# Kernel optimization log

Hardware: AMD Instinct MI355X
Metric: run time of the kernel (lower is better)

## Reference

```python
import jax, jax.numpy as jnp
import numpy as np
from jax.ops import segment_sum

N = 100000      # nodes
E = 1600000     # edges
G = 128         # graphs in batch
D = 128         # input (embedding) dim
H = 128         # hidden dim
WALK = 16       # random-walk length
PED = 16        # PE embed dim
L = 5           # GNN layers
OUT = 10        # classes
EPS = 1e-5      # batchnorm eps


def setup_inputs() -> dict:
    key = jax.random.key(0)
    ks = jax.random.split(key, 32)
    f = lambda k, shp: (jax.random.normal(k, shp, dtype=jnp.float32) * 0.05)
    inp = {
        'x': jnp.zeros((N,), dtype=jnp.int64) if jax.config.jax_enable_x64 else jnp.zeros((N,), dtype=jnp.int32),
        'edge_index': jax.random.randint(ks[0], (2, E), 0, N),
        'batch': jnp.sort(jax.random.randint(ks[1], (N,), 0, G)),
        'emb_table': f(ks[2], (1, D)),
        'pe_w': f(ks[3], (WALK, PED)), 'pe_b': f(ks[4], (PED,)),
        'proj_w': f(ks[5], (D + PED, H)), 'proj_b': f(ks[6], (H,)),
        'gin_w1': f(ks[7], (L, H, H)), 'gin_b1': f(ks[8], (L, H)),
        'gin_w2': f(ks[9], (L, H, H)), 'gin_b2': f(ks[10], (L, H)),
        'bn_g': jnp.ones((L, H), jnp.float32), 'bn_b': jnp.zeros((L, H), jnp.float32),
        'ffn_w1': f(ks[11], (L, H, 2 * H)), 'ffn_b1': f(ks[12], (L, 2 * H)),
        'ffn_w2': f(ks[13], (L, 2 * H, H)), 'ffn_b2': f(ks[14], (L, H)),
        'ffn_bn_g': jnp.ones((L, H), jnp.float32), 'ffn_bn_b': jnp.zeros((L, H), jnp.float32),
        'out_w1': f(ks[15], (H, H)), 'out_b1': f(ks[16], (H,)),
        'out_w2': f(ks[17], (H, OUT)), 'out_b2': f(ks[18], (OUT,)),
    }
    return inp


def _batchnorm(h, g, b):
    # BatchNorm1d forward with batch statistics (training-mode math)
    mu = jnp.mean(h, axis=0)
    var = jnp.var(h, axis=0)
    return (h - mu) * jax.lax.rsqrt(var + EPS) * g + b


def _forward(emb_table, pe_w, pe_b, proj_w, proj_b, gin_w1, gin_b1, gin_w2, gin_b2,
             bn_g, bn_b, ffn_w1, ffn_b1, ffn_w2, ffn_b2, ffn_bn_g, ffn_bn_b,
             out_w1, out_b1, out_w2, out_b2, x, edge_index, batch):
    h0 = emb_table[x]                                # [N, D] (all indices are 0)

    # ---- RandomWalkPositionalEncoding (vectorized scatter-add per step) ----
    row0, col0 = edge_index[0], edge_index[1]
    loops = jnp.arange(N)
    row = jnp.concatenate([row0, loops])
    col = jnp.concatenate([col0, loops])             # self loops appended
    deg = segment_sum(jnp.ones(row.shape, jnp.float32), col, num_segments=N)
    dinv = jnp.where(deg > 0, jax.lax.rsqrt(jnp.maximum(deg, 1.0)), 0.0)
    norm_e = dinv[row] * dinv[col]                   # [E+N]

    cnt = segment_sum(jnp.ones((N,), jnp.float32), batch, num_segments=G)
    prob = 1.0 / jnp.maximum(cnt, 1.0)[batch]        # per-graph uniform init

    def rw_step(p, _):
        new_p = segment_sum(p[row] * norm_e, col, num_segments=N)
        return new_p * 0.9 + p * 0.1, p

    _, rw = jax.lax.scan(rw_step, prob, None, length=WALK)   # [WALK, N]
    pe = rw.T @ pe_w + pe_b                          # [N, PED]

    # ---- input projection ----
    h = jnp.concatenate([h0, pe], axis=-1) @ proj_w + proj_b # [N, H]

    # ---- stacked GIN layers with BN, residual and FFN (dropout = eval identity) ----
    for i in range(L):
        res = h
        agg = segment_sum(h[row0], col0, num_segments=N) + h  # GIN: (1+eps)x + sum_j x_j, eps=0
        z = jax.nn.relu(agg @ gin_w1[i] + gin_b1[i]) @ gin_w2[i] + gin_b2[i]
        z = jax.nn.relu(_batchnorm(z, bn_g[i], bn_b[i]))
        h = z + res
        res2 = h
        f = jax.nn.relu(h @ ffn_w1[i] + ffn_b1[i]) @ ffn_w2[i] + ffn_b2[i]
        h = _batchnorm(f + res2, ffn_bn_g[i], ffn_bn_b[i])

    # ---- global mean pooling + MLP head ----
    gsum = segment_sum(h, batch, num_segments=G)
    g = gsum / jnp.maximum(cnt, 1.0)[:, None]        # [G, H]
    out = jax.nn.relu(g @ out_w1 + out_b1) @ out_w2 + out_b2
    return out                                        # [G, OUT]


def reference(x, edge_index, batch, emb_table, pe_w, pe_b, proj_w, proj_b,
              gin_w1, gin_b1, gin_w2, gin_b2, bn_g, bn_b, ffn_w1, ffn_b1,
              ffn_w2, ffn_b2, ffn_bn_g, ffn_bn_b, out_w1, out_b1, out_w2, out_b2):
    return _forward(emb_table, pe_w, pe_b, proj_w, proj_b, gin_w1, gin_b1, gin_w2,
                    gin_b2, bn_g, bn_b, ffn_w1, ffn_b1, ffn_w2, ffn_b2,
                    ffn_bn_g, ffn_bn_b, out_w1, out_b1, out_w2, out_b2,
                    x, edge_index, batch)
```

## Files before the change

### kernel.cpp

```cpp
#include <hip/hip_runtime.h>
#include <math.h>

#define NN 100000
#define NE 1600000
#define NG 128
#define HD 128
#define WLK 16
#define NL 5
#define NOUT 10
#define BNEPS 1e-5f
#define CDIV(a,b) (((a)+(b)-1)/(b))

#define NBKT 782
#define NEB 400
#define EPB 4000
#define NSCAN (NBKT*NEB)
#define NSB CDIV(NSCAN,1024)
#define NBM 782

typedef float f32x4 __attribute__((ext_vector_type(4)));
typedef _Float16 f16x8 __attribute__((ext_vector_type(8)));
typedef unsigned short ushort_t;
typedef unsigned int uint_t;

__device__ __forceinline__ ushort_t f2h(float x) {
    union { _Float16 h; ushort_t u; } c;
    c.h = (_Float16)x;
    return c.u;
}
__device__ __forceinline__ float h2f(ushort_t u) {
    union { ushort_t u; _Float16 h; } c;
    c.u = u;
    return (float)c.h;
}

__global__ void k_cnt(const int* __restrict__ batch, int* __restrict__ cnt) {
    int g = threadIdx.x;
    if (g >= NG) return;
    int lo0 = 0, hi0 = NN;
    while (lo0 < hi0) { int m = (lo0 + hi0) >> 1; if (batch[m] < g) lo0 = m + 1; else hi0 = m; }
    int lo1 = lo0, hi1 = NN;
    while (lo1 < hi1) { int m = (lo1 + hi1) >> 1; if (batch[m] < g + 1) lo1 = m + 1; else hi1 = m; }
    cnt[g] = lo1 - lo0;
}

__global__ void k_bhist(const int* __restrict__ col0, int* __restrict__ bhist) {
    __shared__ int hist[NBKT];
    for (int i = threadIdx.x; i < NBKT; i += 256) hist[i] = 0;
    __syncthreads();
    int e0 = blockIdx.x * EPB;
    for (int e = e0 + threadIdx.x; e < e0 + EPB; e += 256) atomicAdd(&hist[col0[e] >> 7], 1);
    __syncthreads();
    for (int i = threadIdx.x; i < NBKT; i += 256) bhist[i * NEB + blockIdx.x] = hist[i];
}

__global__ void k_gscan1(const int* __restrict__ in, int* __restrict__ bsum) {
    __shared__ int sm[256];
    int base = blockIdx.x * 1024 + threadIdx.x * 4;
    int s = 0;
#pragma unroll
    for (int i = 0; i < 4; ++i) { int e = base + i; if (e < NSCAN) s += in[e]; }
    sm[threadIdx.x] = s; __syncthreads();
    for (int st = 128; st > 0; st >>= 1) {
        if (threadIdx.x < st) sm[threadIdx.x] += sm[threadIdx.x + st];
        __syncthreads();
    }
    if (threadIdx.x == 0) bsum[blockIdx.x] = sm[0];
}

__global__ void k_scan2(int* __restrict__ blksum, int nblk) {
    __shared__ int sm[512];
    int t = threadIdx.x;
    int x = (t < nblk) ? blksum[t] : 0;
    sm[t] = x; __syncthreads();
    for (int s = 1; s < 512; s <<= 1) {
        int v = (t >= s) ? sm[t - s] : 0;
        __syncthreads();
        sm[t] += v;
        __syncthreads();
    }
    if (t < nblk) blksum[t] = sm[t] - x;
}

__global__ void k_gscan3(const int* __restrict__ in, const int* __restrict__ bsum,
                         int* __restrict__ out) {
    __shared__ int sm[256];
    int t = threadIdx.x;
    int base = blockIdx.x * 1024 + t * 4;
    int v[4]; int s = 0;
#pragma unroll
    for (int i = 0; i < 4; ++i) { int e = base + i; v[i] = (e < NSCAN) ? in[e] : 0; s += v[i]; }
    sm[t] = s; __syncthreads();
    for (int st = 1; st < 256; st <<= 1) {
        int x = (t >= st) ? sm[t - st] : 0;
        __syncthreads();
        sm[t] += x;
        __syncthreads();
    }
    int excl = sm[t] - s + bsum[blockIdx.x];
#pragma unroll
    for (int i = 0; i < 4; ++i) { int e = base + i; if (e < NSCAN) { out[e] = excl; excl += v[i]; } }
}

__global__ void k_escatter(const int* __restrict__ row0, const int* __restrict__ col0,
                           const int* __restrict__ boffs, int2* __restrict__ epair) {
    __shared__ int cur[NBKT];
    for (int i = threadIdx.x; i < NBKT; i += 256) cur[i] = boffs[i * NEB + blockIdx.x];
    __syncthreads();
    int e0 = blockIdx.x * EPB;
    for (int e = e0 + threadIdx.x; e < e0 + EPB; e += 256) {
        int c = col0[e], r = row0[e];
        int pos = atomicAdd(&cur[c >> 7], 1);
        epair[pos] = make_int2(c, r);
    }
}

__global__ void k_bucket(const int2* __restrict__ epair, const int* __restrict__ boffs,
                         int* __restrict__ rowptr, int* __restrict__ deg,
                         int* __restrict__ esrc) {
    __shared__ int cnt_[128], scn[128], cur_[128];
    int bkt = blockIdx.x, t = threadIdx.x;
    int bs = boffs[bkt * NEB];
    int be = (bkt + 1 < NBKT) ? boffs[(bkt + 1) * NEB] : NE;
    if (t < 128) cnt_[t] = 0;
    __syncthreads();
    for (int e = bs + t; e < be; e += 256) atomicAdd(&cnt_[epair[e].x & 127], 1);
    __syncthreads();
    int c = (t < 128) ? cnt_[t] : 0;
    if (t < 128) scn[t] = c;
    __syncthreads();
    for (int st = 1; st < 128; st <<= 1) {
        int x = (t >= st && t < 128) ? scn[t - st] : 0;
        __syncthreads();
        if (t < 128) scn[t] += x;
        __syncthreads();
    }
    if (t < 128) {
        int excl = scn[t] - c;
        int node = bkt * 128 + t;
        if (node < NN) { rowptr[node] = bs + excl; deg[node] = c; }
        cur_[t] = bs + excl;
    }
    if (bkt == NBKT - 1 && t == 0) rowptr[NN] = NE;
    __syncthreads();
    for (int e = bs + t; e < be; e += 256) {
        int2 p = epair[e];
        int pos = atomicAdd(&cur_[p.x & 127], 1);
        esrc[pos] = p.y;
    }
}

__global__ void k_init_pe(const int* __restrict__ deg, const int* __restrict__ batch,
                          const int* __restrict__ cnt, float* __restrict__ dinv,
                          float* __restrict__ p, float* __restrict__ pd) {
    int v = blockIdx.x * 256 + threadIdx.x;
    if (v >= NN) return;
    float dv = rsqrtf((float)(deg[v] + 1));
    dinv[v] = dv;
    float pv = 1.0f / fmaxf((float)cnt[batch[v]], 1.0f);
    p[v] = pv; pd[v] = pv * dv;
}

__global__ void k_rw_step(const float* __restrict__ pin, const float* __restrict__ pdin,
                          const int* __restrict__ rowptr, const int* __restrict__ esrc,
                          const float* __restrict__ dinv, float* __restrict__ rwslice,
                          float* __restrict__ pout, float* __restrict__ pdout) {
    int v = blockIdx.x * 256 + threadIdx.x;
    if (v >= NN) return;
    int b = rowptr[v], e = rowptr[v + 1];
    float a0 = 0.f, a1 = 0.f, a2 = 0.f, a3 = 0.f;
    int i = b;
    for (; i + 4 <= e; i += 4) {
        int s0 = esrc[i], s1 = esrc[i + 1], s2 = esrc[i + 2], s3 = esrc[i + 3];
        a0 += pdin[s0]; a1 += pdin[s1]; a2 += pdin[s2]; a3 += pdin[s3];
    }
    for (; i < e; ++i) a0 += pdin[esrc[i]];
    float s = (a0 + a1) + (a2 + a3);
    float dv = dinv[v];
    float pv = pin[v];
    float np = s * dv + pv * dv * dv;
    float nxt = 0.9f * np + 0.1f * pv;
    rwslice[v] = pv;
    pout[v] = nxt;
    pdout[v] = nxt * dv;
}

__global__ void k_mc1(const float* __restrict__ emb, const float* __restrict__ pe_w,
                      const float* __restrict__ pe_b, const float* __restrict__ proj_w,
                      const float* __restrict__ proj_b, float* __restrict__ M,
                      float* __restrict__ c1) {
    int j = threadIdx.x;
    float c0 = proj_b[j];
    for (int d = 0; d < HD; ++d) c0 += emb[d] * proj_w[d * HD + j];
    for (int w = 0; w < WLK; ++w) c0 += pe_b[w] * proj_w[(HD + w) * HD + j];
    c1[j] = c0;
    for (int s = 0; s < WLK; ++s) {
        float m = 0.f;
        for (int w = 0; w < WLK; ++w) m += pe_w[s * WLK + w] * proj_w[(HD + w) * HD + j];
        M[s * HD + j] = m;
    }
}

__global__ void k_proj(const float* __restrict__ rw, const float* __restrict__ M,
                       const float* __restrict__ c1, float4* __restrict__ h4,
                       uint2* __restrict__ hb4) {
    int idx = blockIdx.x * 256 + threadIdx.x;
    if (idx >= NN * 32) return;
    int v = idx >> 5, cg = (idx & 31) * 4;
    float4 acc = *(const float4*)&c1[cg];
#pragma unroll
    for (int s = 0; s < WLK; ++s) {
        float r = rw[s * NN + v];
        float4 m = *(const float4*)&M[s * HD + cg];
        acc.x += r * m.x; acc.y += r * m.y; acc.z += r * m.z; acc.w += r * m.w;
    }
    h4[idx] = acc;
    hb4[idx] = make_uint2((uint_t)f2h(acc.x) | ((uint_t)f2h(acc.y) << 16),
                          (uint_t)f2h(acc.z) | ((uint_t)f2h(acc.w) << 16));
}

__global__ void k_prepw(const float* __restrict__ g1, const float* __restrict__ g2,
                        const float* __restrict__ f1, const float* __restrict__ f2,
                        ushort_t* __restrict__ wt1, ushort_t* __restrict__ wt2,
                        ushort_t* __restrict__ wt3, ushort_t* __restrict__ wt4) {
    int i = blockIdx.x * 256 + threadIdx.x;
    if (i < 81920) {
        int l = i >> 14, rem = i & 16383, n = rem >> 7, k = rem & 127;
        wt1[i] = f2h(g1[l * 16384 + k * 128 + n]);
    } else if (i < 163840) {
        int j = i - 81920;
        int l = j >> 14, rem = j & 16383, n = rem >> 7, k = rem & 127;
        wt2[j] = f2h(g2[l * 16384 + k * 128 + n]);
    } else if (i < 327680) {
        int j = i - 163840;
        int l = j >> 15, rem = j & 32767, n = rem >> 7, k = rem & 127;
        wt3[j] = f2h(f1[l * 32768 + k * 256 + n]);
    } else {
        int j = i - 327680;
        int l = j >> 15, rem = j & 32767, n = rem >> 8, k = rem & 255;
        wt4[j] = f2h(f2[l * 32768 + k * 128 + n]);
    }
}

__global__ void k_aggb(const uint_t* __restrict__ hb2, const int* __restrict__ rowptr,
                       const int* __restrict__ esrc, uint_t* __restrict__ aggb2) {
    int wave = threadIdx.x >> 6, lane = threadIdx.x & 63;
    int v = blockIdx.x * 4 + wave;
    if (v >= NN) return;
    uint_t u = hb2[(size_t)v * 64 + lane];
    float sx0 = h2f((ushort_t)(u & 0xFFFFu)), sy0 = h2f((ushort_t)(u >> 16));
    float sx1 = 0.f, sy1 = 0.f, sx2 = 0.f, sy2 = 0.f, sx3 = 0.f, sy3 = 0.f;
    int b = rowptr[v], e = rowptr[v + 1];
    int i = b;
    for (; i + 4 <= e; i += 4) {
        int s0 = esrc[i], s1 = esrc[i + 1], s2 = esrc[i + 2], s3 = esrc[i + 3];
        uint_t x0 = hb2[(size_t)s0 * 64 + lane];
        uint_t x1 = hb2[(size_t)s1 * 64 + lane];
        uint_t x2 = hb2[(size_t)s2 * 64 + lane];
        uint_t x3 = hb2[(size_t)s3 * 64 + lane];
        sx0 += h2f((ushort_t)(x0 & 0xFFFFu)); sy0 += h2f((ushort_t)(x0 >> 16));
        sx1 += h2f((ushort_t)(x1 & 0xFFFFu)); sy1 += h2f((ushort_t)(x1 >> 16));
        sx2 += h2f((ushort_t)(x2 & 0xFFFFu)); sy2 += h2f((ushort_t)(x2 >> 16));
        sx3 += h2f((ushort_t)(x3 & 0xFFFFu)); sy3 += h2f((ushort_t)(x3 >> 16));
    }
    for (; i < e; ++i) {
        uint_t x = hb2[(size_t)esrc[i] * 64 + lane];
        sx0 += h2f((ushort_t)(x & 0xFFFFu)); sy0 += h2f((ushort_t)(x >> 16));
    }
    float sx = (sx0 + sx1) + (sx2 + sx3);
    float sy = (sy0 + sy1) + (sy2 + sy3);
    aggb2[(size_t)v * 64 + lane] = (uint_t)f2h(sx) | ((uint_t)f2h(sy) << 16);
}

template <int K, bool RELU, bool OUTH16, bool ADDRES, bool DOSTATS>
__global__ __launch_bounds__(256, 2)
void k_mgemm(const ushort_t* __restrict__ A, const ushort_t* __restrict__ WT,
             const float* __restrict__ bias, ushort_t* __restrict__ Ch,
             float* __restrict__ Cf, const float* __restrict__ res,
             float* __restrict__ partS, float* __restrict__ partQ, int ncols) {
    constexpr int LDK = 72;
    __shared__ ushort_t As[128 * LDK];
    __shared__ ushort_t Ws[128 * LDK];
    __shared__ float sS[128], sQ[128];
    const int tid = threadIdx.x;
    const int w = tid >> 6, l = tid & 63;
    const int lm = l & 15, lq = l >> 4;
    const int rb = (w >> 1) * 64, cbw = (w & 1) * 64;
    const int vr0 = blockIdx.x * 128;
    const int cb = blockIdx.y * 128;
    f32x4 acc[4][4] = {};

    for (int kt = 0; kt < K / 64; ++kt) {
        __syncthreads();
#pragma unroll
        for (int it = 0; it < 4; ++it) {
            int f = it * 256 + tid;
            int row = f >> 3, sl = f & 7;
            uint4 a = make_uint4(0, 0, 0, 0);
            int vr = vr0 + row;
            if (vr < NN) a = *(const uint4*)&A[(size_t)vr * K + kt * 64 + sl * 8];
            *(uint4*)&As[row * LDK + sl * 8] = a;
            uint4 wv = *(const uint4*)&WT[(size_t)(cb + row) * K + kt * 64 + sl * 8];
            *(uint4*)&Ws[row * LDK + sl * 8] = wv;
        }
        __syncthreads();
#pragma unroll
        for (int kk = 0; kk < 64; kk += 32) {
            f16x8 af[4], bf[4];
#pragma unroll
            for (int i = 0; i < 4; ++i)
                af[i] = *(const f16x8*)&As[(rb + i * 16 + lm) * LDK + kk + lq * 8];
#pragma unroll
            for (int j = 0; j < 4; ++j)
                bf[j] = *(const f16x8*)&Ws[(cbw + j * 16 + lm) * LDK + kk + lq * 8];
#pragma unroll
            for (int i = 0; i < 4; ++i)
#pragma unroll
                for (int j = 0; j < 4; ++j)
                    acc[i][j] = __builtin_amdgcn_mfma_f32_16x16x32_f16(af[i], bf[j], acc[i][j], 0, 0, 0);
        }
    }

    float bcol[4];
#pragma unroll
    for (int j = 0; j < 4; ++j) bcol[j] = bias[cb + cbw + j * 16 + lm];
    if (DOSTATS && tid < 128) { sS[tid] = 0.f; sQ[tid] = 0.f; }
    __syncthreads();
    float ls[4] = {0, 0, 0, 0}, lsq[4] = {0, 0, 0, 0};
#pragma unroll
    for (int i = 0; i < 4; ++i) {
#pragma unroll
        for (int r = 0; r < 4; ++r) {
            int vr = vr0 + rb + i * 16 + lq * 4 + r;
            if (vr < NN) {
#pragma unroll
                for (int j = 0; j < 4; ++j) {
                    float x = acc[i][j][r] + bcol[j];
                    if (RELU) x = fmaxf(x, 0.f);
                    int c = cb + cbw + j * 16 + lm;
                    if (ADDRES) x += res[(size_t)vr * ncols + c];
                    if (DOSTATS) { ls[j] += x; lsq[j] += x * x; }
                    if (OUTH16) Ch[(size_t)vr * ncols + c] = f2h(x);
                    else        Cf[(size_t)vr * ncols + c] = x;
                }
            }
        }
    }
    if (DOSTATS) {
#pragma unroll
        for (int j = 0; j < 4; ++j) {
            atomicAdd(&sS[cbw + j * 16 + lm], ls[j]);
            atomicAdd(&sQ[cbw + j * 16 + lm], lsq[j]);
        }
        __syncthreads();
        if (tid < 128) {
            partS[(size_t)(cb + tid) * NBM + blockIdx.x] = sS[tid];
            partQ[(size_t)(cb + tid) * NBM + blockIdx.x] = sQ[tid];
        }
    }
}

__global__ void k_bnparm(const float* __restrict__ partS, const float* __restrict__ partQ,
                         const float* __restrict__ g, const float* __restrict__ b,
                         float* __restrict__ bnA, float* __restrict__ bnB) {
    __shared__ float smS[256], smQ[256];
    int c = blockIdx.x, t = threadIdx.x;
    float s = 0.f, q = 0.f;
    for (int i = t; i < NBM; i += 256) {
        s += partS[(size_t)c * NBM + i];
        q += partQ[(size_t)c * NBM + i];
    }
    smS[t] = s; smQ[t] = q; __syncthreads();
    for (int st = 128; st > 0; st >>= 1) {
        if (t < st) { smS[t] += smS[t + st]; smQ[t] += smQ[t + st]; }
        __syncthreads();
    }
    if (t == 0) {
        float mu = smS[0] * (1.0f / NN);
        float var = smQ[0] * (1.0f / NN) - mu * mu;
        float inv = rsqrtf(var + BNEPS);
        float a = g[c] * inv;
        bnA[c] = a;
        bnB[c] = b[c] - mu * a;
    }
}

__global__ void k_bn_relu_res(const float4* __restrict__ z4, const float* __restrict__ bnA,
                              const float* __restrict__ bnB, float4* __restrict__ h4,
                              uint2* __restrict__ hb4) {
    int idx = blockIdx.x * 256 + threadIdx.x;
    if (idx >= NN * 32) return;
    int cg = (idx & 31) * 4;
    float4 A = *(const float4*)&bnA[cg];
    float4 B = *(const float4*)&bnB[cg];
    float4 z = z4[idx], hv = h4[idx];
    float4 nh;
    nh.x = hv.x + fmaxf(z.x * A.x + B.x, 0.f);
    nh.y = hv.y + fmaxf(z.y * A.y + B.y, 0.f);
    nh.z = hv.z + fmaxf(z.z * A.z + B.z, 0.f);
    nh.w = hv.w + fmaxf(z.w * A.w + B.w, 0.f);
    h4[idx] = nh;
    hb4[idx] = make_uint2((uint_t)f2h(nh.x) | ((uint_t)f2h(nh.y) << 16),
                          (uint_t)f2h(nh.z) | ((uint_t)f2h(nh.w) << 16));
}

__global__ void k_bn(const float4* __restrict__ t4, const float* __restrict__ bnA,
                     const float* __restrict__ bnB, float4* __restrict__ h4,
                     uint2* __restrict__ hb4) {
    int idx = blockIdx.x * 256 + threadIdx.x;
    if (idx >= NN * 32) return;
    int cg = (idx & 31) * 4;
    float4 A = *(const float4*)&bnA[cg];
    float4 B = *(const float4*)&bnB[cg];
    float4 t = t4[idx];
    float4 nh;
    nh.x = t.x * A.x + B.x;
    nh.y = t.y * A.y + B.y;
    nh.z = t.z * A.z + B.z;
    nh.w = t.w * A.w + B.w;
    h4[idx] = nh;
    hb4[idx] = make_uint2((uint_t)f2h(nh.x) | ((uint_t)f2h(nh.y) << 16),
                          (uint_t)f2h(nh.z) | ((uint_t)f2h(nh.w) << 16));
}

__global__ void k_pool(const float* __restrict__ h, const int* __restrict__ batch,
                       float* __restrict__ gsum) {
    int c = threadIdx.x;
    int v0 = blockIdx.x * 256;
    if (v0 >= NN) return;
    int vend = (v0 + 256 < NN) ? v0 + 256 : NN;
    float acc = 0.f;
    int bprev = batch[v0];
    for (int v = v0; v < vend; ++v) {
        int bb = batch[v];
        if (bb != bprev) {
            atomicAdd(&gsum[bprev * HD + c], acc);
            acc = 0.f; bprev = bb;
        }
        acc += h[(size_t)v * HD + c];
    }
    atomicAdd(&gsum[bprev * HD + c], acc);
}

__global__ void k_head(const float* __restrict__ gsum, const int* __restrict__ cnt,
                       const float* __restrict__ w1, const float* __restrict__ b1,
                       const float* __restrict__ w2, const float* __restrict__ b2,
                       float* __restrict__ out) {
    __shared__ float gv[HD], av[HD];
    int gid = blockIdx.x, t = threadIdx.x;
    float c = fmaxf((float)cnt[gid], 1.0f);
    gv[t] = gsum[gid * HD + t] / c;
    __syncthreads();
    float a = b1[t];
    for (int k = 0; k < HD; ++k) a += gv[k] * w1[k * HD + t];
    av[t] = fmaxf(a, 0.f);
    __syncthreads();
    if (t < NOUT) {
        float o = b2[t];
        for (int k = 0; k < HD; ++k) o += av[k] * w2[k * NOUT + t];
        out[gid * NOUT + t] = o;
    }
}

static constexpr size_t AL(size_t x) { return (x + 511) & ~(size_t)511; }
static constexpr size_t OFF_H      = 0;
static constexpr size_t OFF_HB     = OFF_H      + AL((size_t)NN * HD * 4);
static constexpr size_t OFF_BUFF   = OFF_HB     + AL((size_t)NN * HD * 2);
static constexpr size_t OFF_SHARE  = OFF_BUFF   + AL((size_t)NN * HD * 4);
static constexpr size_t SZ_SHARE   = AL((size_t)NN * 256 * 2);
static constexpr size_t OFF_RW     = OFF_SHARE  + SZ_SHARE;
static constexpr size_t OFF_P0     = OFF_RW     + AL((size_t)WLK * NN * 4);
static constexpr size_t OFF_P1     = OFF_P0     + AL((size_t)NN * 4);
static constexpr size_t OFF_PD0    = OFF_P1     + AL((size_t)NN * 4);
static constexpr size_t OFF_PD1    = OFF_PD0    + AL((size_t)NN * 4);
static constexpr size_t OFF_DINV   = OFF_PD1    + AL((size_t)NN * 4);
static constexpr size_t OFF_ESRC   = OFF_DINV   + AL((size_t)NN * 4);
static constexpr size_t OFF_ROWPTR = OFF_ESRC   + AL((size_t)NE * 4);
static constexpr size_t OFF_DEG    = OFF_ROWPTR + AL((size_t)(NN + 1) * 4);
static constexpr size_t OFF_BHIST  = OFF_DEG    + AL((size_t)NN * 4);
static constexpr size_t OFF_BOFFS  = OFF_BHIST  + AL((size_t)NSCAN * 4);
static constexpr size_t OFF_BSUM   = OFF_BOFFS  + AL((size_t)NSCAN * 4);
static constexpr size_t OFF_WT1    = OFF_BSUM   + AL(512 * 4);
static constexpr size_t OFF_WT2    = OFF_WT1    + AL((size_t)5 * 16384 * 2);
static constexpr size_t OFF_WT3    = OFF_WT2    + AL((size_t)5 * 16384 * 2);
static constexpr size_t OFF_WT4    = OFF_WT3    + AL((size_t)5 * 32768 * 2);
static constexpr size_t OFF_PARTS  = OFF_WT4    + AL((size_t)5 * 32768 * 2);
static constexpr size_t OFF_PARTQ  = OFF_PARTS  + AL((size_t)128 * NBM * 4);
static constexpr size_t OFF_BNA    = OFF_PARTQ  + AL((size_t)128 * NBM * 4);
static constexpr size_t OFF_BNB    = OFF_BNA    + AL(128 * 4);
static constexpr size_t OFF_M      = OFF_BNB    + AL(128 * 4);
static constexpr size_t OFF_C1     = OFF_M      + AL((size_t)WLK * HD * 4);
static constexpr size_t OFF_CNT    = OFF_C1     + AL(HD * 4);
static constexpr size_t OFF_GSUM   = OFF_CNT    + AL(NG * 4);
static constexpr size_t ZERO_BYTES = (size_t)NG * HD * 4;

extern "C" void kernel_launch(void* const* d_in, const int* in_sizes, int n_in,
                              void* d_out, int out_size, void* d_ws, size_t ws_size,
                              hipStream_t stream) {
    const int* eidx = (const int*)d_in[1];
    const int* row0 = eidx;
    const int* col0 = eidx + NE;
    const int* batch = (const int*)d_in[2];
    const float* emb = (const float*)d_in[3];
    const float* pe_w = (const float*)d_in[4];
    const float* pe_b = (const float*)d_in[5];
    const float* proj_w = (const float*)d_in[6];
    const float* proj_b = (const float*)d_in[7];
    const float* gin_w1 = (const float*)d_in[8];
    const float* gin_b1 = (const float*)d_in[9];
    const float* gin_w2 = (const float*)d_in[10];
    const float* gin_b2 = (const float*)d_in[11];
    const float* bn_g = (const float*)d_in[12];
    const float* bn_b = (const float*)d_in[13];
    const float* ffn_w1 = (const float*)d_in[14];
    const float* ffn_b1 = (const float*)d_in[15];
    const float* ffn_w2 = (const float*)d_in[16];
    const float* ffn_b2 = (const float*)d_in[17];
    const float* ffn_bn_g = (const float*)d_in[18];
    const float* ffn_bn_b = (const float*)d_in[19];
    const float* out_w1 = (const float*)d_in[20];
    const float* out_b1 = (const float*)d_in[21];
    const float* out_w2 = (const float*)d_in[22];
    const float* out_b2 = (const float*)d_in[23];
    float* out = (float*)d_out;

    char* ws = (char*)d_ws;
    float*    h     = (float*)(ws + OFF_H);
    ushort_t* hb    = (ushort_t*)(ws + OFF_HB);
    float*    bufF  = (float*)(ws + OFF_BUFF);
    ushort_t* f1h   = (ushort_t*)(ws + OFF_SHARE);
    ushort_t* aggh  = (ushort_t*)(ws + OFF_SHARE);
    ushort_t* z1h   = (ushort_t*)(ws + OFF_SHARE + (size_t)NN * HD * 2);
    int2*     epair = (int2*)(ws + OFF_SHARE);
    float*    rw    = (float*)(ws + OFF_RW);
    float*    p0    = (float*)(ws + OFF_P0);
    float*    p1    = (float*)(ws + OFF_P1);
    float*    pd0   = (float*)(ws + OFF_PD0);
    float*    pd1   = (float*)(ws + OFF_PD1);
    float*    dinv  = (float*)(ws + OFF_DINV);
    int*      esrc  = (int*)(ws + OFF_ESRC);
    int*      rowptr= (int*)(ws + OFF_ROWPTR);
    int*      deg   = (int*)(ws + OFF_DEG);
    int*      bhist = (int*)(ws + OFF_BHIST);
    int*      boffs = (int*)(ws + OFF_BOFFS);
    int*      bsum  = (int*)(ws + OFF_BSUM);
    ushort_t* wt1   = (ushort_t*)(ws + OFF_WT1);
    ushort_t* wt2   = (ushort_t*)(ws + OFF_WT2);
    ushort_t* wt3   = (ushort_t*)(ws + OFF_WT3);
    ushort_t* wt4   = (ushort_t*)(ws + OFF_WT4);
    float*    partS = (float*)(ws + OFF_PARTS);
    float*    partQ = (float*)(ws + OFF_PARTQ);
    float*    bnA   = (float*)(ws + OFF_BNA);
    float*    bnB   = (float*)(ws + OFF_BNB);
    float*    M     = (float*)(ws + OFF_M);
    float*    c1    = (float*)(ws + OFF_C1);
    int*      cnt   = (int*)(ws + OFF_CNT);
    float*    gsum  = (float*)(ws + OFF_GSUM);

    const int NB = CDIV(NN, 256);
    const int NBV = CDIV(NN * 32, 256);

    hipMemsetAsync(ws + OFF_GSUM, 0, ZERO_BYTES, stream);

    k_cnt<<<1, 128, 0, stream>>>(batch, cnt);
    k_bhist<<<NEB, 256, 0, stream>>>(col0, bhist);
    k_gscan1<<<NSB, 256, 0, stream>>>(bhist, bsum);
    k_scan2<<<1, 512, 0, stream>>>(bsum, NSB);
    k_gscan3<<<NSB, 256, 0, stream>>>(bhist, bsum, boffs);
    k_escatter<<<NEB, 256, 0, stream>>>(row0, col0, boffs, epair);
    k_bucket<<<NBKT, 256, 0, stream>>>(epair, boffs, rowptr, deg, esrc);

    k_init_pe<<<NB, 256, 0, stream>>>(deg, batch, cnt, dinv, p0, pd0);
    k_mc1<<<1, 128, 0, stream>>>(emb, pe_w, pe_b, proj_w, proj_b, M, c1);
    k_prepw<<<1920, 256, 0, stream>>>(gin_w1, gin_w2, ffn_w1, ffn_w2, wt1, wt2, wt3, wt4);
    for (int s = 0; s < WLK; ++s) {
        const float* pin = (s & 1) ? p1 : p0;
        const float* pdin = (s & 1) ? pd1 : pd0;
        float* pout = (s & 1) ? p0 : p1;
        float* pdout = (s & 1) ? pd0 : pd1;
        k_rw_step<<<NB, 256, 0, stream>>>(pin, pdin, rowptr, esrc, dinv,
                                          rw + (size_t)s * NN, pout, pdout);
    }
    k_proj<<<NBV, 256, 0, stream>>>(rw, M, c1, (float4*)h, (uint2*)hb);

    dim3 g1(NBM, 1), g2(NBM, 2);
    for (int i = 0; i < NL; ++i) {
        k_aggb<<<CDIV(NN, 4), 256, 0, stream>>>((const uint_t*)hb, rowptr, esrc, (uint_t*)aggh);
        k_mgemm<128, true, true, false, false><<<g1, 256, 0, stream>>>(
            aggh, wt1 + (size_t)i * 16384, gin_b1 + i * HD, z1h, nullptr, nullptr,
            nullptr, nullptr, 128);
        k_mgemm<128, false, false, false, true><<<g1, 256, 0, stream>>>(
            z1h, wt2 + (size_t)i * 16384, gin_b2 + i * HD, nullptr, bufF, nullptr,
            partS, partQ, 128);
        k_bnparm<<<128, 256, 0, stream>>>(partS, partQ, bn_g + i * HD, bn_b + i * HD, bnA, bnB);
        k_bn_relu_res<<<NBV, 256, 0, stream>>>(
            (const float4*)bufF, bnA, bnB, (float4*)h, (uint2*)hb);
        k_mgemm<128, true, true, false, false><<<g2, 256, 0, stream>>>(
            hb, wt3 + (size_t)i * 32768, ffn_b1 + i * 256, f1h, nullptr, nullptr,
            nullptr, nullptr, 256);
        k_mgemm<256, false, false, true, true><<<g1, 256, 0, stream>>>(
            f1h, wt4 + (size_t)i * 32768, ffn_b2 + i * HD, nullptr, bufF, h,
            partS, partQ, 128);
        k_bnparm<<<128, 256, 0, stream>>>(partS, partQ, ffn_bn_g + i * HD, ffn_bn_b + i * HD, bnA, bnB);
        k_bn<<<NBV, 256, 0, stream>>>(
            (const float4*)bufF, bnA, bnB, (float4*)h, (uint2*)hb);
    }

    k_pool<<<NB, 128, 0, stream>>>(h, batch, gsum);
    k_head<<<NG, 128, 0, stream>>>(gsum, cnt, out_w1, out_b1, out_w2, out_b2, out);
}
```

Before: 1.682 ms.

## Fuse GIN MLP GEMMs, store pre-BN activations in fp16, rework pooling and aggregation unroll

Merges the two GIN-layer GEMMs into one kernel. The intermediate relu(agg@W1+b1) stays in shared memory, and the kernel emits fp16 output plus BatchNorm partial sums. Pre-BatchNorm tensors for both the GIN and FFN branches are now stored as fp16 instead of fp32, which cuts their memory traffic. The aggregation loop is unrolled to 8 gathers for more memory-level parallelism, and pooling uses per-graph offsets with a block reduction instead of serial per-column scans. The cost is lower precision in the BN inputs and a fused kernel that may run at lower occupancy.

New measurement: 1.620 ms. 3.7% less time.

```diff
diff --git a/kernel.cpp b/kernel.cpp
--- a/kernel.cpp
+++ b/kernel.cpp
@@ -34,7 +34,8 @@
     return (float)c.h;
 }
 
-__global__ void k_cnt(const int* __restrict__ batch, int* __restrict__ cnt) {
+__global__ void k_cnt(const int* __restrict__ batch, int* __restrict__ cnt,
+                      int* __restrict__ goff) {
     int g = threadIdx.x;
     if (g >= NG) return;
     int lo0 = 0, hi0 = NN;
@@ -42,6 +43,7 @@
     int lo1 = lo0, hi1 = NN;
     while (lo1 < hi1) { int m = (lo1 + hi1) >> 1; if (batch[m] < g + 1) lo1 = m + 1; else hi1 = m; }
     cnt[g] = lo1 - lo0;
+    goff[g] = lo0;
 }
 
 __global__ void k_bhist(const int* __restrict__ col0, int* __restrict__ bhist) {
@@ -248,28 +250,162 @@
     int v = blockIdx.x * 4 + wave;
     if (v >= NN) return;
     uint_t u = hb2[(size_t)v * 64 + lane];
-    float sx0 = h2f((ushort_t)(u & 0xFFFFu)), sy0 = h2f((ushort_t)(u >> 16));
-    float sx1 = 0.f, sy1 = 0.f, sx2 = 0.f, sy2 = 0.f, sx3 = 0.f, sy3 = 0.f;
+    float sx[8], sy[8];
+#pragma unroll
+    for (int k = 0; k < 8; ++k) { sx[k] = 0.f; sy[k] = 0.f; }
+    sx[0] = h2f((ushort_t)(u & 0xFFFFu)); sy[0] = h2f((ushort_t)(u >> 16));
     int b = rowptr[v], e = rowptr[v + 1];
     int i = b;
-    for (; i + 4 <= e; i += 4) {
-        int s0 = esrc[i], s1 = esrc[i + 1], s2 = esrc[i + 2], s3 = esrc[i + 3];
-        uint_t x0 = hb2[(size_t)s0 * 64 + lane];
-        uint_t x1 = hb2[(size_t)s1 * 64 + lane];
-        uint_t x2 = hb2[(size_t)s2 * 64 + lane];
-        uint_t x3 = hb2[(size_t)s3 * 64 + lane];
-        sx0 += h2f((ushort_t)(x0 & 0xFFFFu)); sy0 += h2f((ushort_t)(x0 >> 16));
-        sx1 += h2f((ushort_t)(x1 & 0xFFFFu)); sy1 += h2f((ushort_t)(x1 >> 16));
-        sx2 += h2f((ushort_t)(x2 & 0xFFFFu)); sy2 += h2f((ushort_t)(x2 >> 16));
-        sx3 += h2f((ushort_t)(x3 & 0xFFFFu)); sy3 += h2f((ushort_t)(x3 >> 16));
+    for (; i + 8 <= e; i += 8) {
+        int idx[8]; uint_t x[8];
+#pragma unroll
+        for (int k = 0; k < 8; ++k) idx[k] = esrc[i + k];
+#pragma unroll
+        for (int k = 0; k < 8; ++k) x[k] = hb2[(size_t)idx[k] * 64 + lane];
+#pragma unroll
+        for (int k = 0; k < 8; ++k) {
+            sx[k] += h2f((ushort_t)(x[k] & 0xFFFFu));
+            sy[k] += h2f((ushort_t)(x[k] >> 16));
+        }
     }
     for (; i < e; ++i) {
         uint_t x = hb2[(size_t)esrc[i] * 64 + lane];
-        sx0 += h2f((ushort_t)(x & 0xFFFFu)); sy0 += h2f((ushort_t)(x >> 16));
-    }
-    float sx = (sx0 + sx1) + (sx2 + sx3);
-    float sy = (sy0 + sy1) + (sy2 + sy3);
-    aggb2[(size_t)v * 64 + lane] = (uint_t)f2h(sx) | ((uint_t)f2h(sy) << 16);
+        sx[0] += h2f((ushort_t)(x & 0xFFFFu)); sy[0] += h2f((ushort_t)(x >> 16));
+    }
+    float fx = ((sx[0] + sx[1]) + (sx[2] + sx[3])) + ((sx[4] + sx[5]) + (sx[6] + sx[7]));
+    float fy = ((sy[0] + sy[1]) + (sy[2] + sy[3])) + ((sy[4] + sy[5]) + (sy[6] + sy[7]));
+    aggb2[(size_t)v * 64 + lane] = (uint_t)f2h(fx) | ((uint_t)f2h(fy) << 16);
+}
+
+#define GLDK 136
+__global__ __launch_bounds__(256)
+void k_gin(const ushort_t* __restrict__ A, const ushort_t* __restrict__ W1T,
+           const ushort_t* __restrict__ W2T, const float* __restrict__ b1,
+           const float* __restrict__ b2, ushort_t* __restrict__ z2h,
+           float* __restrict__ partS, float* __restrict__ partQ) {
+    __shared__ ushort_t As[128 * GLDK];
+    __shared__ ushort_t Ws[64 * GLDK];
+    __shared__ float sS[128], sQ[128];
+    const int tid = threadIdx.x;
+    const int w = tid >> 6, l = tid & 63;
+    const int lm = l & 15, lq = l >> 4;
+    const int rw0 = w * 32;
+    const int vr0 = blockIdx.x * 128;
+    if (tid < 128) { sS[tid] = 0.f; sQ[tid] = 0.f; }
+
+#pragma unroll
+    for (int it = 0; it < 8; ++it) {
+        int f = it * 256 + tid;
+        int row = f >> 4, sl = f & 15;
+        uint4 a = make_uint4(0, 0, 0, 0);
+        int vr = vr0 + row;
+        if (vr < NN) a = *(const uint4*)&A[(size_t)vr * HD + sl * 8];
+        *(uint4*)&As[row * GLDK + sl * 8] = a;
+    }
+
+    f32x4 z1a[2][2][4] = {};
+    for (int c = 0; c < 2; ++c) {
+        __syncthreads();
+#pragma unroll
+        for (int it = 0; it < 4; ++it) {
+            int f = it * 256 + tid;
+            int row = f >> 4, sl = f & 15;
+            *(uint4*)&Ws[row * GLDK + sl * 8] =
+                *(const uint4*)&W1T[(size_t)(c * 64 + row) * HD + sl * 8];
+        }
+        __syncthreads();
+#pragma unroll
+        for (int kk = 0; kk < 128; kk += 32) {
+            f16x8 af[2], bf[4];
+#pragma unroll
+            for (int i = 0; i < 2; ++i)
+                af[i] = *(const f16x8*)&As[(rw0 + i * 16 + lm) * GLDK + kk + lq * 8];
+#pragma unroll
+            for (int j = 0; j < 4; ++j)
+                bf[j] = *(const f16x8*)&Ws[(j * 16 + lm) * GLDK + kk + lq * 8];
+#pragma unroll
+            for (int i = 0; i < 2; ++i)
+#pragma unroll
+                for (int j = 0; j < 4; ++j)
+                    z1a[c][i][j] = __builtin_amdgcn_mfma_f32_16x16x32_f16(af[i], bf[j], z1a[c][i][j], 0, 0, 0);
+        }
+    }
+    __syncthreads();
+
+#pragma unroll
+    for (int c = 0; c < 2; ++c)
+#pragma unroll
+        for (int j = 0; j < 4; ++j) {
+            int col = c * 64 + j * 16 + lm;
+            float bj = b1[col];
+#pragma unroll
+            for (int i = 0; i < 2; ++i)
+#pragma unroll
+                for (int r = 0; r < 4; ++r) {
+                    int row = rw0 + i * 16 + lq * 4 + r;
+                    As[row * GLDK + col] = f2h(fmaxf(z1a[c][i][j][r] + bj, 0.f));
+                }
+        }
+
+    f32x4 z2a[2][2][4] = {};
+    for (int c2 = 0; c2 < 2; ++c2) {
+        __syncthreads();
+#pragma unroll
+        for (int it = 0; it < 4; ++it) {
+            int f = it * 256 + tid;
+            int row = f >> 4, sl = f & 15;
+            *(uint4*)&Ws[row * GLDK + sl * 8] =
+                *(const uint4*)&W2T[(size_t)(c2 * 64 + row) * HD + sl * 8];
+        }
+        __syncthreads();
+#pragma unroll
+        for (int kk = 0; kk < 128; kk += 32) {
+            f16x8 af[2], bf[4];
+#pragma unroll
+            for (int i = 0; i < 2; ++i)
+                af[i] = *(const f16x8*)&As[(rw0 + i * 16 + lm) * GLDK + kk + lq * 8];
+#pragma unroll
+            for (int j = 0; j < 4; ++j)
+                bf[j] = *(const f16x8*)&Ws[(j * 16 + lm) * GLDK + kk + lq * 8];
+#pragma unroll
+            for (int i = 0; i < 2; ++i)
+#pragma unroll
+                for (int j = 0; j < 4; ++j)
+                    z2a[c2][i][j] = __builtin_amdgcn_mfma_f32_16x16x32_f16(af[i], bf[j], z2a[c2][i][j], 0, 0, 0);
+        }
+    }
+
+    float ls[2][4] = {}, lsq[2][4] = {};
+#pragma unroll
+    for (int c2 = 0; c2 < 2; ++c2)
+#pragma unroll
+        for (int j = 0; j < 4; ++j) {
+            int col = c2 * 64 + j * 16 + lm;
+            float bj = b2[col];
+#pragma unroll
+            for (int i = 0; i < 2; ++i)
+#pragma unroll
+                for (int r = 0; r < 4; ++r) {
+                    int vr = vr0 + rw0 + i * 16 + lq * 4 + r;
+                    if (vr < NN) {
+                        float x = z2a[c2][i][j][r] + bj;
+                        ls[c2][j] += x; lsq[c2][j] += x * x;
+                        z2h[(size_t)vr * HD + col] = f2h(x);
+                    }
+                }
+        }
+#pragma unroll
+    for (int c2 = 0; c2 < 2; ++c2)
+#pragma unroll
+        for (int j = 0; j < 4; ++j) {
+            atomicAdd(&sS[c2 * 64 + j * 16 + lm], ls[c2][j]);
+            atomicAdd(&sQ[c2 * 64 + j * 16 + lm], lsq[c2][j]);
+        }
+    __syncthreads();
+    if (tid < 128) {
+        partS[(size_t)tid * NBM + blockIdx.x] = sS[tid];
+        partQ[(size_t)tid * NBM + blockIdx.x] = sQ[tid];
+    }
 }
 
 template <int K, bool RELU, bool OUTH16, bool ADDRES, bool DOSTATS>
@@ -385,7 +521,7 @@
     }
 }
 
-__global__ void k_bn_relu_res(const float4* __restrict__ z4, const float* __restrict__ bnA,
+__global__ void k_bn_relu_res(const uint2* __restrict__ z4, const float* __restrict__ bnA,
                               const float* __restrict__ bnB, float4* __restrict__ h4,
                               uint2* __restrict__ hb4) {
     int idx = blockIdx.x * 256 + threadIdx.x;
@@ -393,18 +529,21 @@
     int cg = (idx & 31) * 4;
     float4 A = *(const float4*)&bnA[cg];
     float4 B = *(const float4*)&bnB[cg];
-    float4 z = z4[idx], hv = h4[idx];
+    uint2 zv = z4[idx];
+    float z0 = h2f((ushort_t)(zv.x & 0xFFFFu)), z1 = h2f((ushort_t)(zv.x >> 16));
+    float z2 = h2f((ushort_t)(zv.y & 0xFFFFu)), z3 = h2f((ushort_t)(zv.y >> 16));
+    float4 hv = h4[idx];
     float4 nh;
-    nh.x = hv.x + fmaxf(z.x * A.x + B.x, 0.f);
-    nh.y = hv.y + fmaxf(z.y * A.y + B.y, 0.f);
-    nh.z = hv.z + fmaxf(z.z * A.z + B.z, 0.f);
-    nh.w = hv.w + fmaxf(z.w * A.w + B.w, 0.f);
+    nh.x = hv.x + fmaxf(z0 * A.x + B.x, 0.f);
+    nh.y = hv.y + fmaxf(z1 * A.y + B.y, 0.f);
+    nh.z = hv.z + fmaxf(z2 * A.z + B.z, 0.f);
+    nh.w = hv.w + fmaxf(z3 * A.w + B.w, 0.f);
     h4[idx] = nh;
     hb4[idx] = make_uint2((uint_t)f2h(nh.x) | ((uint_t)f2h(nh.y) << 16),
                           (uint_t)f2h(nh.z) | ((uint_t)f2h(nh.w) << 16));
 }
 
-__global__ void k_bn(const float4* __restrict__ t4, const float* __restrict__ bnA,
+__global__ void k_bn(const uint2* __restrict__ t4, const float* __restrict__ bnA,
                      const float* __restrict__ bnB, float4* __restrict__ h4,
                      uint2* __restrict__ hb4) {
     int idx = blockIdx.x * 256 + threadIdx.x;
@@ -412,34 +551,46 @@
     int cg = (idx & 31) * 4;
     float4 A = *(const float4*)&bnA[cg];
     float4 B = *(const float4*)&bnB[cg];
-    float4 t = t4[idx];
+    uint2 tv = t4[idx];
+    float t0 = h2f((ushort_t)(tv.x & 0xFFFFu)), t1 = h2f((ushort_t)(tv.x >> 16));
+    float t2 = h2f((ushort_t)(tv.y & 0xFFFFu)), t3 = h2f((ushort_t)(tv.y >> 16));
     float4 nh;
-    nh.x = t.x * A.x + B.x;
-    nh.y = t.y * A.y + B.y;
-    nh.z = t.z * A.z + B.z;
-    nh.w = t.w * A.w + B.w;
+    nh.x = t0 * A.x + B.x;
+    nh.y = t1 * A.y + B.y;
+    nh.z = t2 * A.z + B.z;
+    nh.w = t3 * A.w + B.w;
     h4[idx] = nh;
     hb4[idx] = make_uint2((uint_t)f2h(nh.x) | ((uint_t)f2h(nh.y) << 16),
                           (uint_t)f2h(nh.z) | ((uint_t)f2h(nh.w) << 16));
 }
 
-__global__ void k_pool(const float* __restrict__ h, const int* __restrict__ batch,
-                       float* __restrict__ gsum) {
-    int c = threadIdx.x;
-    int v0 = blockIdx.x * 256;
-    if (v0 >= NN) return;
-    int vend = (v0 + 256 < NN) ? v0 + 256 : NN;
-    float acc = 0.f;
-    int bprev = batch[v0];
-    for (int v = v0; v < vend; ++v) {
-        int bb = batch[v];
-        if (bb != bprev) {
-            atomicAdd(&gsum[bprev * HD + c], acc);
-            acc = 0.f; bprev = bb;
-        }
-        acc += h[(size_t)v * HD + c];
-    }
-    atomicAdd(&gsum[bprev * HD + c], acc);
+__global__ void k_pool(const float4* __restrict__ h4, const int* __restrict__ goff,
+                       const int* __restrict__ cnt, float* __restrict__ gsum) {
+    __shared__ float4 sm[256];
+    int g = blockIdx.x >> 2, sub = blockIdx.x & 3;
+    int n0 = goff[g], n = cnt[g];
+    int cg = threadIdx.x & 31, rl = threadIdx.x >> 5;
+    float4 acc = make_float4(0.f, 0.f, 0.f, 0.f);
+    for (int r = sub * 8 + rl; r < n; r += 32) {
+        float4 v = h4[(size_t)(n0 + r) * 32 + cg];
+        acc.x += v.x; acc.y += v.y; acc.z += v.z; acc.w += v.w;
+    }
+    sm[threadIdx.x] = acc; __syncthreads();
+    for (int st = 128; st >= 32; st >>= 1) {
+        if (threadIdx.x < st) {
+            float4 o = sm[threadIdx.x + st];
+            sm[threadIdx.x].x += o.x; sm[threadIdx.x].y += o.y;
+            sm[threadIdx.x].z += o.z; sm[threadIdx.x].w += o.w;
+        }
+        __syncthreads();
+    }
+    if (threadIdx.x < 32) {
+        float4 v = sm[threadIdx.x];
+        atomicAdd(&gsum[g * HD + cg * 4 + 0], v.x);
+        atomicAdd(&gsum[g * HD + cg * 4 + 1], v.y);
+        atomicAdd(&gsum[g * HD + cg * 4 + 2], v.z);
+        atomicAdd(&gsum[g * HD + cg * 4 + 3], v.w);
+    }
 }
 
 __global__ void k_head(const float* __restrict__ gsum, const int* __restrict__ cnt,
@@ -491,7 +642,8 @@
 static constexpr size_t OFF_M      = OFF_BNB    + AL(128 * 4);
 static constexpr size_t OFF_C1     = OFF_M      + AL((size_t)WLK * HD * 4);
 static constexpr size_t OFF_CNT    = OFF_C1     + AL(HD * 4);
-static constexpr size_t OFF_GSUM   = OFF_CNT    + AL(NG * 4);
+static constexpr size_t OFF_GOFF   = OFF_CNT    + AL(NG * 4);
+static constexpr size_t OFF_GSUM   = OFF_GOFF   + AL(NG * 4);
 static constexpr size_t ZERO_BYTES = (size_t)NG * HD * 4;
 
 extern "C" void kernel_launch(void* const* d_in, const int* in_sizes, int n_in,
@@ -527,10 +679,10 @@
     char* ws = (char*)d_ws;
     float*    h     = (float*)(ws + OFF_H);
     ushort_t* hb    = (ushort_t*)(ws + OFF_HB);
-    float*    bufF  = (float*)(ws + OFF_BUFF);
+    ushort_t* th    = (ushort_t*)(ws + OFF_BUFF);
+    ushort_t* aggh  = (ushort_t*)(ws + OFF_SHARE);
+    ushort_t* z2h   = (ushort_t*)(ws + OFF_SHARE + (size_t)NN * HD * 2);
     ushort_t* f1h   = (ushort_t*)(ws + OFF_SHARE);
-    ushort_t* aggh  = (ushort_t*)(ws + OFF_SHARE);
-    ushort_t* z1h   = (ushort_t*)(ws + OFF_SHARE + (size_t)NN * HD * 2);
     int2*     epair = (int2*)(ws + OFF_SHARE);
     float*    rw    = (float*)(ws + OFF_RW);
     float*    p0    = (float*)(ws + OFF_P0);
@@ -555,6 +707,7 @@
     float*    M     = (float*)(ws + OFF_M);
     float*    c1    = (float*)(ws + OFF_C1);
     int*      cnt   = (int*)(ws + OFF_CNT);
+    int*      goff  = (int*)(ws + OFF_GOFF);
     float*    gsum  = (float*)(ws + OFF_GSUM);
 
     const int NB = CDIV(NN, 256);
@@ -562,7 +715,7 @@
 
     hipMemsetAsync(ws + OFF_GSUM, 0, ZERO_BYTES, stream);
 
-    k_cnt<<<1, 128, 0, stream>>>(batch, cnt);
+    k_cnt<<<1, 128, 0, stream>>>(batch, cnt, goff);
     k_bhist<<<NEB, 256, 0, stream>>>(col0, bhist);
     k_gscan1<<<NSB, 256, 0, stream>>>(bhist, bsum);
     k_scan2<<<1, 512, 0, stream>>>(bsum, NSB);
@@ -586,26 +739,22 @@
     dim3 g1(NBM, 1), g2(NBM, 2);
     for (int i = 0; i < NL; ++i) {
         k_aggb<<<CDIV(NN, 4), 256, 0, stream>>>((const uint_t*)hb, rowptr, esrc, (uint_t*)aggh);
-        k_mgemm<128, true, true, false, false><<<g1, 256, 0, stream>>>(
-            aggh, wt1 + (size_t)i * 16384, gin_b1 + i * HD, z1h, nullptr, nullptr,
-            nullptr, nullptr, 128);
-        k_mgemm<128, false, false, false, true><<<g1, 256, 0, stream>>>(
-            z1h, wt2 + (size_t)i * 16384, gin_b2 + i * HD, nullptr, bufF, nullptr,
-            partS, partQ, 128);
+        k_gin<<<NBM, 256, 0, stream>>>(aggh, wt1 + (size_t)i * 16384, wt2 + (size_t)i * 16384,
+                                       gin_b1 + i * HD, gin_b2 + i * HD, z2h, partS, partQ);
         k_bnparm<<<128, 256, 0, stream>>>(partS, partQ, bn_g + i * HD, bn_b + i * HD, bnA, bnB);
         k_bn_relu_res<<<NBV, 256, 0, stream>>>(
-            (const float4*)bufF, bnA, bnB, (float4*)h, (uint2*)hb);
+            (const uint2*)z2h, bnA, bnB, (float4*)h, (uint2*)hb);
         k_mgemm<128, true, true, false, false><<<g2, 256, 0, stream>>>(
             hb, wt3 + (size_t)i * 32768, ffn_b1 + i * 256, f1h, nullptr, nullptr,
             nullptr, nullptr, 256);
-        k_mgemm<256, false, false, true, true><<<g1, 256, 0, stream>>>(
-            f1h, wt4 + (size_t)i * 32768, ffn_b2 + i * HD, nullptr, bufF, h,
+        k_mgemm<256, false, true, true, true><<<g1, 256, 0, stream>>>(
+            f1h, wt4 + (size_t)i * 32768, ffn_b2 + i * HD, th, nullptr, h,
             partS, partQ, 128);
         k_bnparm<<<128, 256, 0, stream>>>(partS, partQ, ffn_bn_g + i * HD, ffn_bn_b + i * HD, bnA, bnB);
         k_bn<<<NBV, 256, 0, stream>>>(
-            (const float4*)bufF, bnA, bnB, (float4*)h, (uint2*)hb);
-    }
-
-    k_pool<<<NB, 128, 0, stream>>>(h, batch, gsum);
+            (const uint2*)th, bnA, bnB, (float4*)h, (uint2*)hb);
+    }
+
+    k_pool<<<NG * 4, 256, 0, stream>>>((const float4*)h, goff, cnt, gsum);
     k_head<<<NG, 128, 0, stream>>>(gsum, cnt, out_w1, out_b1, out_w2, out_b2, out);
 }
```
